# Kernel tuning notes

Measured on AMD Instinct MI355X. Metric: run time of the kernel, lower is better.

Reference implementation:

```python
import jax, jax.numpy as jnp
import numpy as np

NEG_INF = -9e15


def setup_inputs() -> dict:
    key = jax.random.key(0)
    k1, k2, k3, k4 = jax.random.split(key, 4)
    N, F_in, H, F_out = 4096, 512, 8, 64
    node_features = jax.random.normal(k1, (N, F_in), dtype=jnp.float32)
    adj_matrix = jax.random.randint(k2, (N, N), 0, 2, dtype=jnp.int32)
    # ensure self-loops so every row has at least one unmasked entry
    adj_matrix = jnp.maximum(adj_matrix, jnp.eye(N, dtype=jnp.int32))
    W = jax.random.normal(k3, (H, F_in, F_out), dtype=jnp.float32) * 0.05
    a = jax.random.normal(k4, (H, 2 * F_out), dtype=jnp.float32) * 0.05
    return {"node_features": node_features, "adj_matrix": adj_matrix, "W": W, "a": a}


def reference(node_features, adj_matrix, W, a):
    alpha = 0.2
    H, F_in, F_out = W.shape
    # Per-head linear projection: [H, N, F_out]
    Wh = jnp.einsum("nf,hfo->hno", node_features, W)
    # Attention logits e_ij = LeakyReLU(a1 . Wh_i + a2 . Wh_j)
    f_src = jnp.einsum("hno,ho->hn", Wh, a[:, :F_out])   # [H, N]
    f_dst = jnp.einsum("hno,ho->hn", Wh, a[:, F_out:])   # [H, N]
    e = jax.nn.leaky_relu(f_src[:, :, None] + f_dst[:, None, :], negative_slope=alpha)  # [H, N, N]
    # Mask by adjacency, softmax over neighbors
    masked = jnp.where(adj_matrix[None, :, :] > 0, e, NEG_INF)
    attn = jax.nn.softmax(masked, axis=-1)               # [H, N, N]
    # Aggregate neighbor features per head
    h_prime = jnp.einsum("hnm,hmo->hno", attn, Wh)       # [H, N, F_out]
    # Concat heads along feature dim -> [N, H*F_out]
    return jnp.transpose(h_prime, (1, 0, 2)).reshape(h_prime.shape[1], H * F_out)
```

## Files before the change

### kernel.cpp

```cpp
#include <hip/hip_runtime.h>
#include <stdint.h>


#define NN 4096
#define FIN 512
#define NH 8
#define FO 64

typedef _Float16 f16x8 __attribute__((ext_vector_type(8)));
typedef _Float16 f16x2 __attribute__((ext_vector_type(2)));
typedef __attribute__((ext_vector_type(4))) float f32x4;

union H8 { f16x8 v; f16x2 p[4]; unsigned u[4]; };
union U2 { unsigned u; f16x2 v; };

#define GLOAD_LDS16(g, l)                                                          \
  __builtin_amdgcn_global_load_lds((__attribute__((address_space(1))) const void*)(g), \
                                   (__attribute__((address_space(3))) void*)(l), 16, 0, 0)
#define GLOAD_LDS4(g, l)                                                           \
  __builtin_amdgcn_global_load_lds((__attribute__((address_space(1))) const void*)(g), \
                                   (__attribute__((address_space(3))) void*)(l), 4, 0, 0)

__device__ __forceinline__ unsigned short f2h(float f) {
  _Float16 h = (_Float16)f;
  return __builtin_bit_cast(unsigned short, h);
}

__global__ __launch_bounds__(256) void prep_kernel(
    const float* __restrict__ X, const int* __restrict__ adj, const float* __restrict__ W,
    const float* __restrict__ a,
    unsigned short* __restrict__ Xh, unsigned short* __restrict__ WbT,
    unsigned* __restrict__ adjbitsT, unsigned short* __restrict__ WAh) {
  int bid = blockIdx.x, tid = threadIdx.x;
  if (bid < 2048) {
    int item = bid * 256 + tid;
    int jt = item >> 12, r = item & 4095;
    const int* p = adj + (size_t)r * NN + jt * 32;
    unsigned bits = 0;
#pragma unroll
    for (int b = 0; b < 32; b += 4) {
      int4 v = *(const int4*)(p + b);
      bits |= (unsigned)(v.x & 1) << b;
      bits |= (unsigned)(v.y & 1) << (b + 1);
      bits |= (unsigned)(v.z & 1) << (b + 2);
      bits |= (unsigned)(v.w & 1) << (b + 3);
    }
    adjbitsT[item] = bits;
  } else if (bid < 4096) {
    int item = (bid - 2048) * 256 + tid;
    float4 v = ((const float4*)X)[item];
    ushort4 o;
    o.x = f2h(v.x); o.y = f2h(v.y); o.z = f2h(v.z); o.w = f2h(v.w);
    ((ushort4*)Xh)[item] = o;
  } else if (bid < 5120) {
    int item = (bid - 4096) * 256 + tid;
    int h = item >> 15, rem = item & 32767, o = rem >> 9, k = rem & 511;
    WbT[item] = f2h(W[h * (FIN * FO) + k * FO + o]);
  } else {
    int item = (bid - 5120) * 256 + tid;
    int h = item >> 10, which = (item >> 9) & 1, k = item & 511;
    const float4* wp = (const float4*)(W + ((size_t)h * FIN + k) * FO);
    const float4* ap = (const float4*)(a + h * 128 + which * 64);
    float s = 0.f;
#pragma unroll
    for (int o4 = 0; o4 < 16; ++o4) {
      float4 w4 = wp[o4], a4 = ap[o4];
      s += w4.x * a4.x + w4.y * a4.y + w4.z * a4.z + w4.w * a4.w;
    }
    WAh[(h * 2 + which) * FIN + k] = f2h(s);
  }
}

__global__ __launch_bounds__(256, 4) void proj_sd_kernel(
    const unsigned short* __restrict__ Xh, const unsigned short* __restrict__ WbT,
    const unsigned short* __restrict__ WAh,
    unsigned short* __restrict__ Whfrag, float2* __restrict__ ABf,
    unsigned short* __restrict__ E1h, unsigned short* __restrict__ E2h) {
  int lane = threadIdx.x & 63, wave = threadIdx.x >> 6;
  int row16 = lane & 15, grp = lane >> 4;
  if (blockIdx.y == 8) {
    int i0 = (blockIdx.x * 4 + wave) * 16;
    f32x4 acc = {0, 0, 0, 0};
    const unsigned short* xb = Xh + (size_t)(i0 + row16) * FIN + grp * 8;
    const unsigned short* wb = WAh + row16 * FIN + grp * 8;
#pragma unroll
    for (int k0 = 0; k0 < FIN; k0 += 32)
      acc = __builtin_amdgcn_mfma_f32_16x16x32_f16(*(const f16x8*)(xb + k0),
                                                   *(const f16x8*)(wb + k0), acc, 0, 0, 0);
    int hh = row16 >> 1;
#pragma unroll
    for (int reg = 0; reg < 4; ++reg) {
      int rr = i0 + grp * 4 + reg;
      float v = acc[reg];
      if (row16 & 1) {
        E1h[hh * NN + rr] = f2h(__expf(v));
        E2h[hh * NN + rr] = f2h(__expf(0.2f * v));
      } else {
        ABf[hh * NN + rr] = make_float2(__expf(v), __expf(0.2f * v));
      }
    }
    return;
  }
  int h = blockIdx.y;
  int i0 = blockIdx.x * 64 + wave * 16;
  f32x4 acc[4] = {{0,0,0,0},{0,0,0,0},{0,0,0,0},{0,0,0,0}};
  const unsigned short* xb = Xh + (size_t)(i0 + row16) * FIN + grp * 8;
  const unsigned short* wb = WbT + h * (FO * FIN) + row16 * FIN + grp * 8;
#pragma unroll 4
  for (int k0 = 0; k0 < FIN; k0 += 32) {
    f16x8 af = *(const f16x8*)(xb + k0);
#pragma unroll
    for (int cb = 0; cb < 4; ++cb)
      acc[cb] = __builtin_amdgcn_mfma_f32_16x16x32_f16(
          af, *(const f16x8*)(wb + cb * 16 * FIN + k0), acc[cb], 0, 0, 0);
  }
  int jt = i0 >> 5;
  int kk0 = (i0 & 31) + grp * 4;
  int tl = (kk0 >> 3) * 16 + row16;
  int e0 = kk0 & 7;
#pragma unroll
  for (int cb = 0; cb < 4; ++cb) {
    ushort4 pk;
    pk.x = f2h(acc[cb][0]); pk.y = f2h(acc[cb][1]);
    pk.z = f2h(acc[cb][2]); pk.w = f2h(acc[cb][3]);
    *(ushort4*)(Whfrag + (((size_t)h * 128 + jt) * 4 + cb) * 512 + tl * 8 + e0) = pk;
  }
}

#define SEGB 9216
#define E_OFF 8192
#define A_OFF 8448
#define PH 2
#define NPHASE 32

__global__ __launch_bounds__(512, 8) void gat_kernel(
    const unsigned* __restrict__ adjbitsT, const unsigned short* __restrict__ Whfrag,
    const float2* __restrict__ ABf, const unsigned short* __restrict__ E1h,
    const unsigned short* __restrict__ E2h, float* __restrict__ out) {
  __shared__ __align__(16) char lds[4 * SEGB];
  int h = blockIdx.y;
  int lane = threadIdx.x & 63, wave = threadIdx.x >> 6;
  int row16 = lane & 15, grp = lane >> 4;
  int rt = wave >> 1, jseg = wave & 1;
  int r0 = blockIdx.x * 64;
  int i0 = r0 + rt * 16;
  int r = i0 + row16;
  float2 ab = ABf[h * NN + r];
  _Float16 Ah1 = (_Float16)(0.5f * ab.x);
  _Float16 Bh1 = (_Float16)(0.5f * ab.y);
  f16x2 Ah = {Ah1, Ah1}, Bh = {Bh1, Bh1};

  H8 ones;
#pragma unroll
  for (int k = 0; k < 4; ++k) ones.u[k] = 0x3C003C00u;

  const unsigned short* wsrc = Whfrag + (size_t)h * 262144 + lane * 8;
  const unsigned short* e1src = E1h + h * NN + jseg * 2048 + lane * 8;
  const unsigned short* e2src = E2h + h * NN + jseg * 2048 + lane * 8;

  f32x4 a0 = {0,0,0,0}, a1 = {0,0,0,0}, a2 = {0,0,0,0}, ad = {0,0,0,0}, aden = {0,0,0,0};

  auto stage = [&](int buf, int p) {
    char* base = lds + (jseg * 2 + buf) * SEGB;
    int jt0 = jseg * 64 + p * PH;
    if (rt < 2) {
      const unsigned short* bs = wsrc + (size_t)(jt0 + rt) * 2048;
      char* bd = base + rt * 4096;
      GLOAD_LDS16(bs, bd);
      GLOAD_LDS16(bs + 512, bd + 1024);
      GLOAD_LDS16(bs + 1024, bd + 2048);
      GLOAD_LDS16(bs + 1536, bd + 3072);
    } else {
      int t = rt - 2;
      GLOAD_LDS4(adjbitsT + (size_t)(jt0 + t) * NN + r0 + lane, base + A_OFF + t * 256);
      if (lane < 8) {
        const unsigned short* es = (t == 0 ? e1src : e2src) + p * (PH * 32);
        GLOAD_LDS16(es, base + E_OFF + t * 128);
      }
    }
  };

  auto compute = [&](int buf) {
    char* base = lds + (jseg * 2 + buf) * SEGB;
#pragma unroll
    for (int t = 0; t < PH; ++t) {
      unsigned bw = *(const unsigned*)(base + A_OFF + t * 256 + (rt * 16 + row16) * 4);
      unsigned bb = (bw >> (grp * 8)) & 0xffu;
      H8 e1, e2;
      e1.v = *(const f16x8*)(base + E_OFF + t * 64 + grp * 16);
      e2.v = *(const f16x8*)(base + E_OFF + 128 + t * 64 + grp * 16);
      const char* bbase = base + t * 4096 + lane * 16;
      f16x8 b0 = *(const f16x8*)(bbase);
      f16x8 b1 = *(const f16x8*)(bbase + 1024);
      f16x8 b2 = *(const f16x8*)(bbase + 2048);
      f16x8 b3 = *(const f16x8*)(bbase + 3072);
      H8 af;
#pragma unroll
      for (int k = 0; k < 4; ++k) {
        f16x2 mx = __builtin_elementwise_max(Ah * e1.p[k], Bh * e2.p[k]);
        U2 m;
        m.u = (((bb >> (2 * k)) & 1u) << 14) | (((bb >> (2 * k + 1)) & 1u) << 30);
        af.p[k] = mx * m.v;
      }
      a0   = __builtin_amdgcn_mfma_f32_16x16x32_f16(af.v, b0, a0, 0, 0, 0);
      a1   = __builtin_amdgcn_mfma_f32_16x16x32_f16(af.v, b1, a1, 0, 0, 0);
      a2   = __builtin_amdgcn_mfma_f32_16x16x32_f16(af.v, b2, a2, 0, 0, 0);
      aden = __builtin_amdgcn_mfma_f32_16x16x32_f16(af.v, ones.v, aden, 0, 0, 0);
      ad   = __builtin_amdgcn_mfma_f32_16x16x32_f16(af.v, b3, ad, 0, 0, 0);
    }
  };

  stage(0, 0);
  __syncthreads();
  int b = 0;
#pragma unroll 1
  for (int p = 0; p < NPHASE; ++p) {
    if (p < NPHASE - 1) stage(b ^ 1, p + 1);
    compute(b);
    __syncthreads();
    b ^= 1;
  }

  float* red = (float*)lds;
  if (jseg == 1) {
    float* q = red + (rt * 64 + lane) * 20;
    *(f32x4*)(q +  0) = a0;
    *(f32x4*)(q +  4) = a1;
    *(f32x4*)(q +  8) = a2;
    *(f32x4*)(q + 12) = ad;
    *(f32x4*)(q + 16) = aden;
  }
  __syncthreads();
  if (jseg == 0) {
    const float* q = red + (rt * 64 + lane) * 20;
    a0   += *(const f32x4*)(q +  0);
    a1   += *(const f32x4*)(q +  4);
    a2   += *(const f32x4*)(q +  8);
    ad   += *(const f32x4*)(q + 12);
    aden += *(const f32x4*)(q + 16);
#pragma unroll
    for (int reg = 0; reg < 4; ++reg) {
      float inv = 1.0f / aden[reg];
      int row = i0 + grp * 4 + reg;
      float* op = out + (size_t)row * (NH * FO) + h * FO + row16;
      op[0]  = a0[reg] * inv;
      op[16] = a1[reg] * inv;
      op[32] = a2[reg] * inv;
      op[48] = ad[reg] * inv;
    }
  }
}

extern "C" void kernel_launch(void* const* d_in, const int* in_sizes, int n_in,
                              void* d_out, int out_size, void* d_ws, size_t ws_size,
                              hipStream_t stream) {
  const float* X  = (const float*)d_in[0];
  const int* adj  = (const int*)d_in[1];
  const float* W  = (const float*)d_in[2];
  const float* a  = (const float*)d_in[3];
  float* out = (float*)d_out;
  char* ws = (char*)d_ws;

  unsigned short* Xh     = (unsigned short*)(ws + 0);
  unsigned short* WbT    = (unsigned short*)(ws + 4194304);
  unsigned* adjbitsT     = (unsigned*)(ws + 4718592);
  unsigned short* Whfrag = (unsigned short*)(ws + 6815744);
  unsigned short* WAh    = (unsigned short*)(ws + 11010048);
  float2* ABf            = (float2*)(ws + 11026432);
  unsigned short* E1h    = (unsigned short*)(ws + 11288576);
  unsigned short* E2h    = (unsigned short*)(ws + 11354112);

  prep_kernel<<<5152, 256, 0, stream>>>(X, adj, W, a, Xh, WbT, adjbitsT, WAh);
  proj_sd_kernel<<<dim3(64, 9), 256, 0, stream>>>(Xh, WbT, WAh, Whfrag, ABf, E1h, E2h);
  gat_kernel<<<dim3(64, 8), 512, 0, stream>>>(adjbitsT, Whfrag, ABf, E1h, E2h, out);
}
```

Measured before the change: 82.03 us.

## Split neighbor dimension four ways with smaller row tiles in GAT aggregation

Each block now covers 32 rows instead of 64, and its 8 waves split the 4096 neighbors into four segments instead of two. This doubles the grid to 1024 blocks for better CU occupancy and load balance. Each stage holds one 32-column tile per segment, and the loop is manually unrolled over two fixed LDS buffers. The mask bits are extracted with a cheaper shift-and-mask. In exchange, the Wh fragments are reloaded twice as often across blocks, and the cross-segment reduction through LDS grows from one partial to three.

```diff
diff --git a/kernel.cpp b/kernel.cpp
--- a/kernel.cpp
+++ b/kernel.cpp
@@ -127,22 +127,20 @@
   }
 }
 
-#define SEGB 9216
-#define E_OFF 8192
-#define A_OFF 8448
-#define PH 2
-#define NPHASE 32
+#define SEGB 4608
+#define E_OFF 4096
+#define A_OFF 4224
 
 __global__ __launch_bounds__(512, 8) void gat_kernel(
     const unsigned* __restrict__ adjbitsT, const unsigned short* __restrict__ Whfrag,
     const float2* __restrict__ ABf, const unsigned short* __restrict__ E1h,
     const unsigned short* __restrict__ E2h, float* __restrict__ out) {
-  __shared__ __align__(16) char lds[4 * SEGB];
+  __shared__ __align__(16) char lds[8 * SEGB];
   int h = blockIdx.y;
   int lane = threadIdx.x & 63, wave = threadIdx.x >> 6;
   int row16 = lane & 15, grp = lane >> 4;
-  int rt = wave >> 1, jseg = wave & 1;
-  int r0 = blockIdx.x * 64;
+  int rt = wave >> 2, jseg = wave & 3;
+  int r0 = blockIdx.x * 32;
   int i0 = r0 + rt * 16;
   int r = i0 + row16;
   float2 ab = ABf[h * NN + r];
@@ -154,76 +152,71 @@
 #pragma unroll
   for (int k = 0; k < 4; ++k) ones.u[k] = 0x3C003C00u;
 
-  const unsigned short* wsrc = Whfrag + (size_t)h * 262144 + lane * 8;
-  const unsigned short* e1src = E1h + h * NN + jseg * 2048 + lane * 8;
-  const unsigned short* e2src = E2h + h * NN + jseg * 2048 + lane * 8;
+  const unsigned short* wsrc =
+      Whfrag + (size_t)h * 262144 + (size_t)jseg * 32 * 2048 + lane * 8;
+  const unsigned short* esrc =
+      ((lane & 4) ? E2h : E1h) + h * NN + jseg * 1024 + (lane & 3) * 8;
+  const unsigned* asrc = adjbitsT + (size_t)(jseg * 32) * NN + r0 + lane;
 
   f32x4 a0 = {0,0,0,0}, a1 = {0,0,0,0}, a2 = {0,0,0,0}, ad = {0,0,0,0}, aden = {0,0,0,0};
 
-  auto stage = [&](int buf, int p) {
-    char* base = lds + (jseg * 2 + buf) * SEGB;
-    int jt0 = jseg * 64 + p * PH;
-    if (rt < 2) {
-      const unsigned short* bs = wsrc + (size_t)(jt0 + rt) * 2048;
-      char* bd = base + rt * 4096;
-      GLOAD_LDS16(bs, bd);
-      GLOAD_LDS16(bs + 512, bd + 1024);
-      GLOAD_LDS16(bs + 1024, bd + 2048);
-      GLOAD_LDS16(bs + 1536, bd + 3072);
+  char* seg0 = lds + (jseg * 2 + 0) * SEGB;
+  char* seg1 = lds + (jseg * 2 + 1) * SEGB;
+
+  auto stage = [&](char* seg, int p) {
+    if (rt == 0) {
+      const unsigned short* bs = wsrc + (size_t)p * 2048;
+      GLOAD_LDS16(bs, seg);
+      GLOAD_LDS16(bs + 512, seg + 1024);
+      GLOAD_LDS16(bs + 1024, seg + 2048);
+      GLOAD_LDS16(bs + 1536, seg + 3072);
     } else {
-      int t = rt - 2;
-      GLOAD_LDS4(adjbitsT + (size_t)(jt0 + t) * NN + r0 + lane, base + A_OFF + t * 256);
-      if (lane < 8) {
-        const unsigned short* es = (t == 0 ? e1src : e2src) + p * (PH * 32);
-        GLOAD_LDS16(es, base + E_OFF + t * 128);
-      }
+      if (lane < 32) GLOAD_LDS4(asrc + (size_t)p * NN, seg + A_OFF);
+      if (lane < 8)  GLOAD_LDS16(esrc + p * 32, seg + E_OFF);
     }
   };
 
-  auto compute = [&](int buf) {
-    char* base = lds + (jseg * 2 + buf) * SEGB;
-#pragma unroll
-    for (int t = 0; t < PH; ++t) {
-      unsigned bw = *(const unsigned*)(base + A_OFF + t * 256 + (rt * 16 + row16) * 4);
-      unsigned bb = (bw >> (grp * 8)) & 0xffu;
-      H8 e1, e2;
-      e1.v = *(const f16x8*)(base + E_OFF + t * 64 + grp * 16);
-      e2.v = *(const f16x8*)(base + E_OFF + 128 + t * 64 + grp * 16);
-      const char* bbase = base + t * 4096 + lane * 16;
-      f16x8 b0 = *(const f16x8*)(bbase);
-      f16x8 b1 = *(const f16x8*)(bbase + 1024);
-      f16x8 b2 = *(const f16x8*)(bbase + 2048);
-      f16x8 b3 = *(const f16x8*)(bbase + 3072);
-      H8 af;
-#pragma unroll
-      for (int k = 0; k < 4; ++k) {
-        f16x2 mx = __builtin_elementwise_max(Ah * e1.p[k], Bh * e2.p[k]);
-        U2 m;
-        m.u = (((bb >> (2 * k)) & 1u) << 14) | (((bb >> (2 * k + 1)) & 1u) << 30);
-        af.p[k] = mx * m.v;
-      }
-      a0   = __builtin_amdgcn_mfma_f32_16x16x32_f16(af.v, b0, a0, 0, 0, 0);
-      a1   = __builtin_amdgcn_mfma_f32_16x16x32_f16(af.v, b1, a1, 0, 0, 0);
-      a2   = __builtin_amdgcn_mfma_f32_16x16x32_f16(af.v, b2, a2, 0, 0, 0);
-      aden = __builtin_amdgcn_mfma_f32_16x16x32_f16(af.v, ones.v, aden, 0, 0, 0);
-      ad   = __builtin_amdgcn_mfma_f32_16x16x32_f16(af.v, b3, ad, 0, 0, 0);
-    }
+  auto compute = [&](const char* seg) {
+    unsigned bw = *(const unsigned*)(seg + A_OFF + (rt * 16 + row16) * 4);
+    unsigned bb = (bw >> (grp * 8)) & 0xffu;
+    unsigned t32 = bb | (bb << 15);
+    H8 e1, e2;
+    e1.v = *(const f16x8*)(seg + E_OFF + grp * 16);
+    e2.v = *(const f16x8*)(seg + E_OFF + 64 + grp * 16);
+    const char* bp = seg + lane * 16;
+    f16x8 b0 = *(const f16x8*)(bp);
+    f16x8 b1 = *(const f16x8*)(bp + 1024);
+    f16x8 b2 = *(const f16x8*)(bp + 2048);
+    f16x8 b3 = *(const f16x8*)(bp + 3072);
+    H8 af;
+#pragma unroll
+    for (int k = 0; k < 4; ++k) {
+      U2 m;
+      m.u = (t32 << (14 - 2 * k)) & 0x40004000u;
+      af.p[k] = __builtin_elementwise_max(Ah * e1.p[k], Bh * e2.p[k]) * m.v;
+    }
+    a0   = __builtin_amdgcn_mfma_f32_16x16x32_f16(af.v, b0, a0, 0, 0, 0);
+    a1   = __builtin_amdgcn_mfma_f32_16x16x32_f16(af.v, b1, a1, 0, 0, 0);
+    a2   = __builtin_amdgcn_mfma_f32_16x16x32_f16(af.v, b2, a2, 0, 0, 0);
+    aden = __builtin_amdgcn_mfma_f32_16x16x32_f16(af.v, ones.v, aden, 0, 0, 0);
+    ad   = __builtin_amdgcn_mfma_f32_16x16x32_f16(af.v, b3, ad, 0, 0, 0);
   };
 
-  stage(0, 0);
+  stage(seg0, 0);
   __syncthreads();
-  int b = 0;
 #pragma unroll 1
-  for (int p = 0; p < NPHASE; ++p) {
-    if (p < NPHASE - 1) stage(b ^ 1, p + 1);
-    compute(b);
+  for (int p2 = 0; p2 < 16; ++p2) {
+    stage(seg1, 2 * p2 + 1);
+    compute(seg0);
     __syncthreads();
-    b ^= 1;
+    if (p2 < 15) stage(seg0, 2 * p2 + 2);
+    compute(seg1);
+    __syncthreads();
   }
 
   float* red = (float*)lds;
-  if (jseg == 1) {
-    float* q = red + (rt * 64 + lane) * 20;
+  if (jseg != 0) {
+    float* q = red + (((jseg - 1) * 2 + rt) * 64 + lane) * 20;
     *(f32x4*)(q +  0) = a0;
     *(f32x4*)(q +  4) = a1;
     *(f32x4*)(q +  8) = a2;
@@ -232,12 +225,15 @@
   }
   __syncthreads();
   if (jseg == 0) {
-    const float* q = red + (rt * 64 + lane) * 20;
-    a0   += *(const f32x4*)(q +  0);
-    a1   += *(const f32x4*)(q +  4);
-    a2   += *(const f32x4*)(q +  8);
-    ad   += *(const f32x4*)(q + 12);
-    aden += *(const f32x4*)(q + 16);
+#pragma unroll
+    for (int s = 0; s < 3; ++s) {
+      const float* q = red + ((s * 2 + rt) * 64 + lane) * 20;
+      a0   += *(const f32x4*)(q +  0);
+      a1   += *(const f32x4*)(q +  4);
+      a2   += *(const f32x4*)(q +  8);
+      ad   += *(const f32x4*)(q + 12);
+      aden += *(const f32x4*)(q + 16);
+    }
 #pragma unroll
     for (int reg = 0; reg < 4; ++reg) {
       float inv = 1.0f / aden[reg];
@@ -272,5 +268,5 @@
 
   prep_kernel<<<5152, 256, 0, stream>>>(X, adj, W, a, Xh, WbT, adjbitsT, WAh);
   proj_sd_kernel<<<dim3(64, 9), 256, 0, stream>>>(Xh, WbT, WAh, Whfrag, ABf, E1h, E2h);
-  gat_kernel<<<dim3(64, 8), 512, 0, stream>>>(adjbitsT, Whfrag, ABf, E1h, E2h, out);
-}
+  gat_kernel<<<dim3(128, 8), 512, 0, stream>>>(adjbitsT, Whfrag, ABf, E1h, E2h, out);
+}
```

Result: slower. 84.69 us (+3.2%).
